# Optimization experiments

Measured on AMD Instinct MI355X. Metric: run time of the kernel, lower is better.

Reference implementation:

```python
import jax, jax.numpy as jnp
import numpy as np

D_MODEL = 2048
N_HEADS = 32
N_KV = 8
HEAD_DIM = D_MODEL // N_HEADS        # 64
N_GROUPS = N_HEADS // N_KV           # 4
ROPE_BASE = 10000.0
SCALE = HEAD_DIM ** -0.5
BATCH, SEQ = 2, 2048


def setup_inputs() -> dict:
    key = jax.random.key(0)
    k1, k2, k3, k4, k5 = jax.random.split(key, 5)
    init = 0.02  # typical transformer init scale
    return {
        "x":  jax.random.normal(k1, (BATCH, SEQ, D_MODEL), jnp.float32),
        "Wq": jax.random.normal(k2, (D_MODEL, D_MODEL), jnp.float32) * init,
        "Wk": jax.random.normal(k3, (N_KV * HEAD_DIM, D_MODEL), jnp.float32) * init,
        "Wv": jax.random.normal(k4, (N_KV * HEAD_DIM, D_MODEL), jnp.float32) * init,
        "Wo": jax.random.normal(k5, (D_MODEL, D_MODEL), jnp.float32) * init,
    }


def _apply_rope(q, k, seq_len):
    # q: (b, n_heads, s, hd), k: (b, n_kv, s, hd). LLaMA-style rotate-half RoPE.
    half = HEAD_DIM // 2
    inv_freq = 1.0 / (ROPE_BASE ** (jnp.arange(0, half, dtype=jnp.float32) / half))
    ang = jnp.arange(seq_len, dtype=jnp.float32)[:, None] * inv_freq[None, :]  # (s, half)
    cos = jnp.concatenate([jnp.cos(ang), jnp.cos(ang)], axis=-1)[None, None]   # (1,1,s,hd)
    sin = jnp.concatenate([jnp.sin(ang), jnp.sin(ang)], axis=-1)[None, None]

    def rot_half(t):
        t1, t2 = jnp.split(t, 2, axis=-1)
        return jnp.concatenate([-t2, t1], axis=-1)

    q = q * cos + rot_half(q) * sin
    k = k * cos + rot_half(k) * sin
    return q, k


def reference(x, Wq, Wk, Wv, Wo):
    b, s, _ = x.shape
    # projections (nn.Linear: y = x @ W.T)
    q = jnp.einsum('bsd,ed->bse', x, Wq).reshape(b, s, N_HEADS, HEAD_DIM).transpose(0, 2, 1, 3)
    k = jnp.einsum('bsd,ed->bse', x, Wk).reshape(b, s, N_KV, HEAD_DIM).transpose(0, 2, 1, 3)
    v = jnp.einsum('bsd,ed->bse', x, Wv).reshape(b, s, N_KV, HEAD_DIM).transpose(0, 2, 1, 3)

    q, k = _apply_rope(q, k, s)

    # GQA: repeat_interleave(k, n_groups) maps q-head h -> kv-head h // n_groups,
    # equivalent to grouping consecutive q heads and broadcasting kv per group.
    qg = q.reshape(b, N_KV, N_GROUPS, s, HEAD_DIM)
    scores = jnp.einsum('bkgqd,bkld->bkgql', qg, k) * SCALE   # (b, n_kv, g, s, s)
    attn = jax.nn.softmax(scores, axis=-1)
    out = jnp.einsum('bkgql,bkld->bkgqd', attn, v)            # (b, n_kv, g, s, hd)

    out = out.reshape(b, N_HEADS, s, HEAD_DIM).transpose(0, 2, 1, 3).reshape(b, s, D_MODEL)
    return jnp.einsum('bsd,ed->bse', out, Wo)
```

## Files before the change

### kernel.cpp

```cpp
#include <hip/hip_runtime.h>
#include <hip/hip_bf16.h>


typedef __attribute__((ext_vector_type(8))) short short8;
typedef __attribute__((ext_vector_type(4))) float f32x4;
typedef __attribute__((ext_vector_type(16))) float f32x16;

#define MFMA16(A, B, C) __builtin_amdgcn_mfma_f32_16x16x32_bf16((A), (B), (C), 0, 0, 0)
#define MFMA32(A, B, C) __builtin_amdgcn_mfma_f32_32x32x16_bf16((A), (B), (C), 0, 0, 0)

__device__ __forceinline__ ushort f2bf(float f) {
  __hip_bfloat16 h = __float2bfloat16(f);
  return __builtin_bit_cast(ushort, h);
}

__device__ __forceinline__ void gload_lds16(const void* g, void* l) {
  __builtin_amdgcn_global_load_lds(
      (const __attribute__((address_space(1))) unsigned int*)g,
      (__attribute__((address_space(3))) unsigned int*)l, 16, 0, 0);
}

__global__ __launch_bounds__(256) void prep_kernel(
    const float* __restrict__ x, const float* __restrict__ Wq,
    const float* __restrict__ Wk, const float* __restrict__ Wv,
    const float* __restrict__ Wo, ushort* __restrict__ xbf,
    ushort* __restrict__ wqbf, ushort* __restrict__ wkbf,
    ushort* __restrict__ wvbf, ushort* __restrict__ wobf,
    float* __restrict__ tc, float* __restrict__ ts) {
  const int blk = blockIdx.x;
  if (blk < 9216) {
    const float* src;
    ushort* dst;
    int t;
    if (blk < 4096) {
      src = x; dst = xbf; t = blk * 256 + threadIdx.x;
    } else if (blk < 6144) {
      src = Wq; dst = wqbf; t = (blk - 4096) * 256 + threadIdx.x;
    } else if (blk < 6656) {
      src = Wk; dst = wkbf; t = (blk - 6144) * 256 + threadIdx.x;
    } else if (blk < 7168) {
      src = Wv; dst = wvbf; t = (blk - 6656) * 256 + threadIdx.x;
    } else {
      src = Wo; dst = wobf; t = (blk - 7168) * 256 + threadIdx.x;
    }
    const float4* p = (const float4*)src;
    float4 a = p[t * 2], b = p[t * 2 + 1];
    int4 o;
    o.x = (int)f2bf(a.x) | ((int)f2bf(a.y) << 16);
    o.y = (int)f2bf(a.z) | ((int)f2bf(a.w) << 16);
    o.z = (int)f2bf(b.x) | ((int)f2bf(b.y) << 16);
    o.w = (int)f2bf(b.z) | ((int)f2bf(b.w) << 16);
    ((int4*)dst)[t] = o;
  } else {
    int t = (blk - 9216) * 256 + threadIdx.x;
    int j = t & 31, s = t >> 5;
    float freq = powf(10000.0f, -(float)j * (1.0f / 32.0f));
    float ang = (float)s * freq;
    tc[t] = cosf(ang);
    ts[t] = sinf(ang);
  }
}

__device__ __forceinline__ void gemm_core(const ushort* __restrict__ A,
                                          const ushort* __restrict__ Bt,
                                          int row0, int col0, int K,
                                          f32x4 (&acc)[4][4]) {
  __shared__ __align__(16) ushort As[8192];
  __shared__ __align__(16) ushort Bs[8192];
  const int t = threadIdx.x;
  const int lane = t & 63, wid = t >> 6;
  const int lr = lane & 15, lh = lane >> 4;
  const int wm = wid >> 1, wn = wid & 1;
#pragma unroll
  for (int i = 0; i < 4; ++i)
#pragma unroll
    for (int j = 0; j < 4; ++j) acc[i][j] = (f32x4){0.f, 0.f, 0.f, 0.f};

  const int srow = t >> 3, scg = (t & 7) ^ (srow & 7);
  const ushort* Asrc = A + (size_t)(row0 + srow) * K + scg * 8;
  const ushort* Bsrc = Bt + (size_t)(col0 + srow) * K + scg * 8;
  char* AsB = (char*)As + wid * 1024;
  char* BsB = (char*)Bs + wid * 1024;
  const int s7a = lr & 7;

  for (int k0 = 0; k0 < K; k0 += 64) {
    __syncthreads();
#pragma unroll
    for (int i = 0; i < 4; ++i) {
      gload_lds16(Asrc + (size_t)(32 * i) * K + k0, AsB + i * 4096);
      gload_lds16(Bsrc + (size_t)(32 * i) * K + k0, BsB + i * 4096);
    }
    __syncthreads();

    short8 af[4][2];
#pragma unroll
    for (int fm = 0; fm < 4; ++fm)
#pragma unroll
      for (int kk = 0; kk < 2; ++kk)
        af[fm][kk] = *(const short8*)((const char*)As +
                                      ((wm * 64 + fm * 16 + lr) << 7) +
                                      (((kk * 4 + lh) ^ s7a) << 4));
#pragma unroll
    for (int kk = 0; kk < 2; ++kk)
#pragma unroll
      for (int fn = 0; fn < 4; ++fn) {
        short8 bf_ = *(const short8*)((const char*)Bs +
                                      ((wn * 64 + fn * 16 + lr) << 7) +
                                      (((kk * 4 + lh) ^ s7a) << 4));
#pragma unroll
        for (int fm = 0; fm < 4; ++fm)
          acc[fm][fn] = MFMA16(af[fm][kk], bf_, acc[fm][fn]);
      }
  }
}

__global__ __launch_bounds__(256) void gemm_qkv_kernel(
    const ushort* __restrict__ xbf, const ushort* __restrict__ wq,
    const ushort* __restrict__ wk, const ushort* __restrict__ wv,
    ushort* __restrict__ Qo, ushort* __restrict__ Ko, ushort* __restrict__ Vo,
    const float* __restrict__ tabc, const float* __restrict__ tabs) {
  int bx = blockIdx.x % 24, by = blockIdx.x / 24;
  const ushort* Bt;
  int cb;
  if (bx < 16) {
    Bt = wq; cb = bx;
  } else if (bx < 20) {
    Bt = wk; cb = bx - 16;
  } else {
    Bt = wv; cb = bx - 20;
  }
  f32x4 acc[4][4];
  gemm_core(xbf, Bt, by * 128, cb * 128, 2048, acc);

  const int lane = threadIdx.x & 63, wid = threadIdx.x >> 6;
  const int lr = lane & 15, lh = lane >> 4;
  const int wm = wid >> 1, wn = wid & 1;
  const int srow0 = by * 128 + wm * 64 + lh * 4;

  if (bx >= 20) {
    const int kv = cb * 2 + wn;
#pragma unroll
    for (int fm = 0; fm < 4; ++fm) {
      int srow = srow0 + fm * 16;
      int bb = srow >> 11, s = srow & 2047;
#pragma unroll
      for (int fn = 0; fn < 4; ++fn) {
        int d = fn * 16 + lr;
        ushort4 o;
        o.x = f2bf(acc[fm][fn][0]);
        o.y = f2bf(acc[fm][fn][1]);
        o.z = f2bf(acc[fm][fn][2]);
        o.w = f2bf(acc[fm][fn][3]);
        *(ushort4*)&Vo[((size_t)((bb * 8 + kv) * 64 + d)) * 2048 + s] = o;
      }
    }
  } else {
    ushort* dst;
    int nh, h;
    float scale;
    if (bx < 16) {
      dst = Qo; nh = 32; h = bx * 2 + wn;
      scale = 0.125f * 1.44269504088896340736f;
    } else {
      dst = Ko; nh = 8; h = cb * 2 + wn; scale = 1.0f;
    }
#pragma unroll
    for (int fm = 0; fm < 4; ++fm) {
      int srow = srow0 + fm * 16;
      int bb = srow >> 11, sbase = srow & 2047;
      size_t obase = (size_t)(bb * nh + h) * 2048;
#pragma unroll
      for (int fn = 0; fn < 2; ++fn) {
        int j = fn * 16 + lr;
#pragma unroll
        for (int r = 0; r < 4; ++r) {
          int s = sbase + r;
          float c = tabc[s * 32 + j], sn = tabs[s * 32 + j];
          float x1 = acc[fm][fn][r], x2 = acc[fm][fn + 2][r];
          ushort* po = &dst[(obase + s) * 64 + j];
          po[0] = f2bf((x1 * c - x2 * sn) * scale);
          po[32] = f2bf((x2 * c + x1 * sn) * scale);
        }
      }
    }
  }
}

__global__ __launch_bounds__(256) void gemm_o_kernel(const ushort* __restrict__ A,
                                                     const ushort* __restrict__ Wo,
                                                     float* __restrict__ C) {
  int bx = blockIdx.x & 15, by = blockIdx.x >> 4;
  int row0 = by * 128, col0 = bx * 128;
  f32x4 acc[4][4];
  gemm_core(A, Wo, row0, col0, 2048, acc);
  const int lane = threadIdx.x & 63, wid = threadIdx.x >> 6;
  const int lr = lane & 15, lh = lane >> 4;
  const int wm = wid >> 1, wn = wid & 1;
#pragma unroll
  for (int fm = 0; fm < 4; ++fm) {
    int r0 = row0 + wm * 64 + fm * 16 + lh * 4;
#pragma unroll
    for (int fn = 0; fn < 4; ++fn) {
      int cc = col0 + wn * 64 + fn * 16 + lr;
#pragma unroll
      for (int r = 0; r < 4; ++r) C[(size_t)(r0 + r) * 2048 + cc] = acc[fm][fn][r];
    }
  }
}

__global__ __launch_bounds__(256, 4) void attn_kernel(const ushort* __restrict__ Q,
                                                      const ushort* __restrict__ Kg,
                                                      const ushort* __restrict__ Vt,
                                                      ushort* __restrict__ O) {
  __shared__ __align__(16) char smem_c[32768];
  const int tid = threadIdx.x;
  const int lane = tid & 63;
  const int wid = tid >> 6;
  const int bid = ((blockIdx.x & 7) << 7) | (blockIdx.x >> 3);
  const int qp = bid & 63;
  const int kvh = (bid >> 6) & 7;
  const int b = bid >> 9;
  const int h = kvh * 4 + wid;
  const int q0 = qp * 32;
  const int l31 = lane & 31;
  const int hi = lane >> 5;

  const ushort* Qp = Q + ((size_t)((b * 32 + h) * 2048 + q0)) * 64;
  const ushort* Kp = Kg + ((size_t)((b * 8 + kvh) * 2048)) * 64;
  const ushort* Vp = Vt + ((size_t)((b * 8 + kvh) * 64)) * 2048;

  const int srow = tid >> 3, scg = (tid & 7) ^ (srow & 7);
  const ushort* Kst = Kp + (size_t)srow * 64 + scg * 8;
  const ushort* Vst = Vp + (size_t)srow * 2048 + scg * 8;

#define STAGE(PAR, KV0)                                                         \
  do {                                                                          \
    char* kd_ = smem_c + (PAR) * 8192 + wid * 1024;                             \
    char* vd_ = smem_c + 16384 + (PAR) * 8192 + wid * 1024;                     \
    gload_lds16(Kst + (size_t)(KV0) * 64, kd_);                                 \
    gload_lds16(Kst + (size_t)((KV0) + 32) * 64, kd_ + 4096);                   \
    gload_lds16(Vst + (KV0), vd_);                                              \
    gload_lds16(Vst + 32 * 2048 + (KV0), vd_ + 4096);                           \
  } while (0)

  STAGE(0, 0);

  const short8 qf0 = *(const short8*)(Qp + (size_t)l31 * 64 + 0 + hi * 8);
  const short8 qf1 = *(const short8*)(Qp + (size_t)l31 * 64 + 16 + hi * 8);
  const short8 qf2 = *(const short8*)(Qp + (size_t)l31 * 64 + 32 + hi * 8);
  const short8 qf3 = *(const short8*)(Qp + (size_t)l31 * 64 + 48 + hi * 8);

  const int s7 = l31 & 7;
  const int ok0 = l31 * 128 + (((0 + hi) ^ s7) << 4);
  const int ok1 = l31 * 128 + (((2 + hi) ^ s7) << 4);
  const int ok2 = l31 * 128 + (((4 + hi) ^ s7) << 4);
  const int ok3 = l31 * 128 + (((6 + hi) ^ s7) << 4);

  f32x16 acc0, acc1, kz;
#pragma unroll
  for (int r = 0; r < 16; ++r) {
    acc0[r] = 0.f;
    acc1[r] = 0.f;
    kz[r] = 0.f;
  }
  float lsh = 0.f;

#define QK(ST, KOFF)                                         \
  do {                                                       \
    const char* kb_ = smem_c + (KOFF);                       \
    short8 kf_ = *(const short8*)(kb_ + ok0);                \
    __builtin_amdgcn_s_setprio(1);                           \
    ST = MFMA32(kf_, qf0, kz);                               \
    kf_ = *(const short8*)(kb_ + ok1);                       \
    ST = MFMA32(kf_, qf1, ST);                               \
    kf_ = *(const short8*)(kb_ + ok2);                       \
    ST = MFMA32(kf_, qf2, ST);                               \
    kf_ = *(const short8*)(kb_ + ok3);                       \
    ST = MFMA32(kf_, qf3, ST);                               \
    __builtin_amdgcn_s_setprio(0);                           \
  } while (0)

#define SMPV(ST, VOFF, VSX)                                                   \
  do {                                                                        \
    float ps_ = 0.f;                                                          \
    uint pk0_, pk1_, pk2_, pk3_, pk4_, pk5_, pk6_, pk7_;                      \
    _Pragma("unroll") for (int j = 0; j < 8; ++j) {                           \
      float pa_ = exp2f(ST[2 * j]);                                           \
      float pb_ = exp2f(ST[2 * j + 1]);                                       \
      ps_ += pa_ + pb_;                                                       \
      uint w_ = __builtin_amdgcn_perm(__builtin_bit_cast(uint, pb_),          \
                                      __builtin_bit_cast(uint, pa_),          \
                                      0x07060302u);                           \
      switch (j) {                                                            \
        case 0: pk0_ = w_; break;                                             \
        case 1: pk1_ = w_; break;                                             \
        case 2: pk2_ = w_; break;                                             \
        case 3: pk3_ = w_; break;                                             \
        case 4: pk4_ = w_; break;                                             \
        case 5: pk5_ = w_; break;                                             \
        case 6: pk6_ = w_; break;                                             \
        default: pk7_ = w_; break;                                            \
      }                                                                       \
    }                                                                         \
    lsh += ps_;                                                               \
    uint u0_ = hi ? pk0_ : pk2_; u0_ = __shfl_xor(u0_, 32);                   \
    uint u1_ = hi ? pk1_ : pk3_; u1_ = __shfl_xor(u1_, 32);                   \
    uint u2_ = hi ? pk4_ : pk6_; u2_ = __shfl_xor(u2_, 32);                   \
    uint u3_ = hi ? pk5_ : pk7_; u3_ = __shfl_xor(u3_, 32);                   \
    union { uint u[4]; short8 s; } f0_, f1_;                                  \
    f0_.u[0] = hi ? u0_ : pk0_;                                               \
    f0_.u[1] = hi ? u1_ : pk1_;                                               \
    f0_.u[2] = hi ? pk2_ : u0_;                                               \
    f0_.u[3] = hi ? pk3_ : u1_;                                               \
    f1_.u[0] = hi ? u2_ : pk4_;                                               \
    f1_.u[1] = hi ? u3_ : pk5_;                                               \
    f1_.u[2] = hi ? pk6_ : u2_;                                               \
    f1_.u[3] = hi ? pk7_ : u3_;                                               \
    const char* vb_ = smem_c + (VOFF);                                        \
    short8 v0_ = *(const short8*)(vb_ + (ok0 ^ (VSX)));                       \
    short8 v1_ = *(const short8*)(vb_ + (ok1 ^ (VSX)));                       \
    __builtin_amdgcn_s_setprio(1);                                            \
    acc0 = MFMA32(v0_, f0_.s, acc0);                                          \
    acc0 = MFMA32(v1_, f1_.s, acc0);                                          \
    __builtin_amdgcn_s_setprio(0);                                            \
    v0_ = *(const short8*)(vb_ + (ok0 ^ (VSX)) + 4096);                       \
    v1_ = *(const short8*)(vb_ + (ok1 ^ (VSX)) + 4096);                       \
    __builtin_amdgcn_s_setprio(1);                                            \
    acc1 = MFMA32(v0_, f0_.s, acc1);                                          \
    acc1 = MFMA32(v1_, f1_.s, acc1);                                          \
    __builtin_amdgcn_s_setprio(0);                                            \
  } while (0)

  for (int t = 0; t < 32; ++t) {
    asm volatile("s_waitcnt vmcnt(0)" ::: "memory");
    __builtin_amdgcn_s_barrier();
    if (t < 31) STAGE((t + 1) & 1, (t + 1) * 64);
    {
      const int kb = (t & 1) * 8192;
      const int vb = 16384 + (t & 1) * 8192;
      f32x16 st0_, st1_;
      QK(st0_, kb);
      QK(st1_, kb + 4096);
      SMPV(st0_, vb, 0);
      SMPV(st1_, vb, 64);
    }
  }
#undef STAGE
#undef QK
#undef SMPV

  float ls = lsh + __shfl_xor(lsh, 32);
  float inv = 1.0f / ls;
  ushort* Ob = O + (size_t)(b * 2048 + q0 + l31) * 2048 + h * 64;
#pragma unroll
  for (int rg = 0; rg < 4; ++rg) {
    ushort4 o0, o1;
    o0.x = f2bf(acc0[rg * 4 + 0] * inv);
    o0.y = f2bf(acc0[rg * 4 + 1] * inv);
    o0.z = f2bf(acc0[rg * 4 + 2] * inv);
    o0.w = f2bf(acc0[rg * 4 + 3] * inv);
    o1.x = f2bf(acc1[rg * 4 + 0] * inv);
    o1.y = f2bf(acc1[rg * 4 + 1] * inv);
    o1.z = f2bf(acc1[rg * 4 + 2] * inv);
    o1.w = f2bf(acc1[rg * 4 + 3] * inv);
    *(ushort4*)(Ob + rg * 8 + hi * 4) = o0;
    *(ushort4*)(Ob + 32 + rg * 8 + hi * 4) = o1;
  }
}

extern "C" void kernel_launch(void* const* d_in, const int* in_sizes, int n_in,
                              void* d_out, int out_size, void* d_ws, size_t ws_size,
                              hipStream_t stream) {
  (void)in_sizes; (void)n_in; (void)out_size; (void)ws_size;
  const float* x = (const float*)d_in[0];
  const float* Wq = (const float*)d_in[1];
  const float* Wk = (const float*)d_in[2];
  const float* Wv = (const float*)d_in[3];
  const float* Wo = (const float*)d_in[4];
  float* out = (float*)d_out;

  char* ws = (char*)d_ws;
  size_t off = 0;
  auto take = [&](size_t bytes) {
    void* p = ws + off;
    off += (bytes + 255) & ~(size_t)255;
    return p;
  };
  ushort* xbf = (ushort*)take(16777216);
  ushort* wqbf = (ushort*)take(8388608);
  ushort* wkbf = (ushort*)take(2097152);
  ushort* wvbf = (ushort*)take(2097152);
  ushort* wobf = (ushort*)take(8388608);
  ushort* Qbf = (ushort*)take(16777216);
  ushort* Kbf = (ushort*)take(4194304);
  ushort* Vtb = (ushort*)take(4194304);
  ushort* attnout = (ushort*)take(16777216);
  float* tabc = (float*)take(262144);
  float* tabs = (float*)take(262144);

  prep_kernel<<<9472, 256, 0, stream>>>(x, Wq, Wk, Wv, Wo, xbf, wqbf, wkbf,
                                        wvbf, wobf, tabc, tabs);
  gemm_qkv_kernel<<<768, 256, 0, stream>>>(xbf, wqbf, wkbf, wvbf, Qbf, Kbf,
                                           Vtb, tabc, tabs);
  attn_kernel<<<1024, 256, 0, stream>>>(Qbf, Kbf, Vtb, attnout);
  gemm_o_kernel<<<512, 256, 0, stream>>>(attnout, wobf, out);
}
```

Measured before the change: 241.8 us.

## Process two 32-row query tiles per wave to reuse K/V tiles

Each attention block now covers 64 query rows instead of 32, so every wave keeps two sets of Q fragments and accumulators and reuses each K and V LDS fragment for both. This halves the grid and halves the K/V global-to-LDS staging per query row. In exchange register pressure roughly doubles, so launch bounds drop to 2 blocks per SM, cutting occupancy. The softmax exp2 also switches to the raw hardware exp instruction.

```diff
diff --git a/kernel.cpp b/kernel.cpp
--- a/kernel.cpp
+++ b/kernel.cpp
@@ -12,6 +12,16 @@
 __device__ __forceinline__ ushort f2bf(float f) {
   __hip_bfloat16 h = __float2bfloat16(f);
   return __builtin_bit_cast(ushort, h);
+}
+
+__device__ __forceinline__ float fexp2(float x) {
+#if __has_builtin(__builtin_amdgcn_exp2f)
+  return __builtin_amdgcn_exp2f(x);
+#else
+  float r;
+  asm("v_exp_f32 %0, %1" : "=v"(r) : "v"(x));
+  return r;
+#endif
 }
 
 __device__ __forceinline__ void gload_lds16(const void* g, void* l) {
@@ -208,7 +218,7 @@
   }
 }
 
-__global__ __launch_bounds__(256, 4) void attn_kernel(const ushort* __restrict__ Q,
+__global__ __launch_bounds__(256, 2) void attn_kernel(const ushort* __restrict__ Q,
                                                       const ushort* __restrict__ Kg,
                                                       const ushort* __restrict__ Vt,
                                                       ushort* __restrict__ O) {
@@ -216,12 +226,12 @@
   const int tid = threadIdx.x;
   const int lane = tid & 63;
   const int wid = tid >> 6;
-  const int bid = ((blockIdx.x & 7) << 7) | (blockIdx.x >> 3);
-  const int qp = bid & 63;
-  const int kvh = (bid >> 6) & 7;
-  const int b = bid >> 9;
+  const int bid = ((blockIdx.x & 7) << 6) | (blockIdx.x >> 3);
+  const int qp = bid & 31;
+  const int kvh = (bid >> 5) & 7;
+  const int b = bid >> 8;
   const int h = kvh * 4 + wid;
-  const int q0 = qp * 32;
+  const int q0 = qp * 64;
   const int l31 = lane & 31;
   const int hi = lane >> 5;
 
@@ -245,10 +255,14 @@
 
   STAGE(0, 0);
 
-  const short8 qf0 = *(const short8*)(Qp + (size_t)l31 * 64 + 0 + hi * 8);
-  const short8 qf1 = *(const short8*)(Qp + (size_t)l31 * 64 + 16 + hi * 8);
-  const short8 qf2 = *(const short8*)(Qp + (size_t)l31 * 64 + 32 + hi * 8);
-  const short8 qf3 = *(const short8*)(Qp + (size_t)l31 * 64 + 48 + hi * 8);
+  const short8 qfA0 = *(const short8*)(Qp + (size_t)l31 * 64 + 0 + hi * 8);
+  const short8 qfA1 = *(const short8*)(Qp + (size_t)l31 * 64 + 16 + hi * 8);
+  const short8 qfA2 = *(const short8*)(Qp + (size_t)l31 * 64 + 32 + hi * 8);
+  const short8 qfA3 = *(const short8*)(Qp + (size_t)l31 * 64 + 48 + hi * 8);
+  const short8 qfB0 = *(const short8*)(Qp + (size_t)(32 + l31) * 64 + 0 + hi * 8);
+  const short8 qfB1 = *(const short8*)(Qp + (size_t)(32 + l31) * 64 + 16 + hi * 8);
+  const short8 qfB2 = *(const short8*)(Qp + (size_t)(32 + l31) * 64 + 32 + hi * 8);
+  const short8 qfB3 = *(const short8*)(Qp + (size_t)(32 + l31) * 64 + 48 + hi * 8);
 
   const int s7 = l31 & 7;
   const int ok0 = l31 * 128 + (((0 + hi) ^ s7) << 4);
@@ -256,37 +270,43 @@
   const int ok2 = l31 * 128 + (((4 + hi) ^ s7) << 4);
   const int ok3 = l31 * 128 + (((6 + hi) ^ s7) << 4);
 
-  f32x16 acc0, acc1, kz;
+  f32x16 accA0, accA1, accB0, accB1, kz;
 #pragma unroll
   for (int r = 0; r < 16; ++r) {
-    acc0[r] = 0.f;
-    acc1[r] = 0.f;
+    accA0[r] = 0.f;
+    accA1[r] = 0.f;
+    accB0[r] = 0.f;
+    accB1[r] = 0.f;
     kz[r] = 0.f;
   }
-  float lsh = 0.f;
-
-#define QK(ST, KOFF)                                         \
+  float lshA = 0.f, lshB = 0.f;
+
+#define QK2(STA, STB, KOFF)                                  \
   do {                                                       \
     const char* kb_ = smem_c + (KOFF);                       \
     short8 kf_ = *(const short8*)(kb_ + ok0);                \
     __builtin_amdgcn_s_setprio(1);                           \
-    ST = MFMA32(kf_, qf0, kz);                               \
+    STA = MFMA32(kf_, qfA0, kz);                             \
+    STB = MFMA32(kf_, qfB0, kz);                             \
     kf_ = *(const short8*)(kb_ + ok1);                       \
-    ST = MFMA32(kf_, qf1, ST);                               \
+    STA = MFMA32(kf_, qfA1, STA);                            \
+    STB = MFMA32(kf_, qfB1, STB);                            \
     kf_ = *(const short8*)(kb_ + ok2);                       \
-    ST = MFMA32(kf_, qf2, ST);                               \
+    STA = MFMA32(kf_, qfA2, STA);                            \
+    STB = MFMA32(kf_, qfB2, STB);                            \
     kf_ = *(const short8*)(kb_ + ok3);                       \
-    ST = MFMA32(kf_, qf3, ST);                               \
+    STA = MFMA32(kf_, qfA3, STA);                            \
+    STB = MFMA32(kf_, qfB3, STB);                            \
     __builtin_amdgcn_s_setprio(0);                           \
   } while (0)
 
-#define SMPV(ST, VOFF, VSX)                                                   \
+#define SMX(ST, F0, F1, LSH)                                                  \
   do {                                                                        \
     float ps_ = 0.f;                                                          \
     uint pk0_, pk1_, pk2_, pk3_, pk4_, pk5_, pk6_, pk7_;                      \
     _Pragma("unroll") for (int j = 0; j < 8; ++j) {                           \
-      float pa_ = exp2f(ST[2 * j]);                                           \
-      float pb_ = exp2f(ST[2 * j + 1]);                                       \
+      float pa_ = fexp2(ST[2 * j]);                                           \
+      float pb_ = fexp2(ST[2 * j + 1]);                                       \
       ps_ += pa_ + pb_;                                                       \
       uint w_ = __builtin_amdgcn_perm(__builtin_bit_cast(uint, pb_),          \
                                       __builtin_bit_cast(uint, pa_),          \
@@ -302,33 +322,43 @@
         default: pk7_ = w_; break;                                            \
       }                                                                       \
     }                                                                         \
-    lsh += ps_;                                                               \
+    LSH += ps_;                                                               \
     uint u0_ = hi ? pk0_ : pk2_; u0_ = __shfl_xor(u0_, 32);                   \
     uint u1_ = hi ? pk1_ : pk3_; u1_ = __shfl_xor(u1_, 32);                   \
     uint u2_ = hi ? pk4_ : pk6_; u2_ = __shfl_xor(u2_, 32);                   \
     uint u3_ = hi ? pk5_ : pk7_; u3_ = __shfl_xor(u3_, 32);                   \
-    union { uint u[4]; short8 s; } f0_, f1_;                                  \
-    f0_.u[0] = hi ? u0_ : pk0_;                                               \
-    f0_.u[1] = hi ? u1_ : pk1_;                                               \
-    f0_.u[2] = hi ? pk2_ : u0_;                                               \
-    f0_.u[3] = hi ? pk3_ : u1_;                                               \
-    f1_.u[0] = hi ? u2_ : pk4_;                                               \
-    f1_.u[1] = hi ? u3_ : pk5_;                                               \
-    f1_.u[2] = hi ? pk6_ : u2_;                                               \
-    f1_.u[3] = hi ? pk7_ : u3_;                                               \
-    const char* vb_ = smem_c + (VOFF);                                        \
-    short8 v0_ = *(const short8*)(vb_ + (ok0 ^ (VSX)));                       \
-    short8 v1_ = *(const short8*)(vb_ + (ok1 ^ (VSX)));                       \
-    __builtin_amdgcn_s_setprio(1);                                            \
-    acc0 = MFMA32(v0_, f0_.s, acc0);                                          \
-    acc0 = MFMA32(v1_, f1_.s, acc0);                                          \
-    __builtin_amdgcn_s_setprio(0);                                            \
-    v0_ = *(const short8*)(vb_ + (ok0 ^ (VSX)) + 4096);                       \
-    v1_ = *(const short8*)(vb_ + (ok1 ^ (VSX)) + 4096);                       \
-    __builtin_amdgcn_s_setprio(1);                                            \
-    acc1 = MFMA32(v0_, f0_.s, acc1);                                          \
-    acc1 = MFMA32(v1_, f1_.s, acc1);                                          \
-    __builtin_amdgcn_s_setprio(0);                                            \
+    F0.u[0] = hi ? u0_ : pk0_;                                                \
+    F0.u[1] = hi ? u1_ : pk1_;                                                \
+    F0.u[2] = hi ? pk2_ : u0_;                                                \
+    F0.u[3] = hi ? pk3_ : u1_;                                                \
+    F1.u[0] = hi ? u2_ : pk4_;                                                \
+    F1.u[1] = hi ? u3_ : pk5_;                                                \
+    F1.u[2] = hi ? pk6_ : u2_;                                                \
+    F1.u[3] = hi ? pk7_ : u3_;                                                \
+  } while (0)
+
+#define SMPV2(STA, STB, VOFF, VSX)                                           \
+  do {                                                                       \
+    union { uint u[4]; short8 s; } fA0_, fA1_, fB0_, fB1_;                   \
+    SMX(STA, fA0_, fA1_, lshA);                                              \
+    SMX(STB, fB0_, fB1_, lshB);                                              \
+    const char* vb_ = smem_c + (VOFF);                                       \
+    short8 v0_ = *(const short8*)(vb_ + (ok0 ^ (VSX)));                      \
+    short8 v1_ = *(const short8*)(vb_ + (ok1 ^ (VSX)));                      \
+    __builtin_amdgcn_s_setprio(1);                                           \
+    accA0 = MFMA32(v0_, fA0_.s, accA0);                                      \
+    accA0 = MFMA32(v1_, fA1_.s, accA0);                                      \
+    accB0 = MFMA32(v0_, fB0_.s, accB0);                                      \
+    accB0 = MFMA32(v1_, fB1_.s, accB0);                                      \
+    __builtin_amdgcn_s_setprio(0);                                           \
+    v0_ = *(const short8*)(vb_ + (ok0 ^ (VSX)) + 4096);                      \
+    v1_ = *(const short8*)(vb_ + (ok1 ^ (VSX)) + 4096);                      \
+    __builtin_amdgcn_s_setprio(1);                                           \
+    accA1 = MFMA32(v0_, fA0_.s, accA1);                                      \
+    accA1 = MFMA32(v1_, fA1_.s, accA1);                                      \
+    accB1 = MFMA32(v0_, fB0_.s, accB1);                                      \
+    accB1 = MFMA32(v1_, fB1_.s, accB1);                                      \
+    __builtin_amdgcn_s_setprio(0);                                           \
   } while (0)
 
   for (int t = 0; t < 32; ++t) {
@@ -338,33 +368,47 @@
     {
       const int kb = (t & 1) * 8192;
       const int vb = 16384 + (t & 1) * 8192;
-      f32x16 st0_, st1_;
-      QK(st0_, kb);
-      QK(st1_, kb + 4096);
-      SMPV(st0_, vb, 0);
-      SMPV(st1_, vb, 64);
+      f32x16 stA0_, stB0_, stA1_, stB1_;
+      QK2(stA0_, stB0_, kb);
+      QK2(stA1_, stB1_, kb + 4096);
+      SMPV2(stA0_, stB0_, vb, 0);
+      SMPV2(stA1_, stB1_, vb, 64);
     }
   }
 #undef STAGE
-#undef QK
-#undef SMPV
-
-  float ls = lsh + __shfl_xor(lsh, 32);
-  float inv = 1.0f / ls;
-  ushort* Ob = O + (size_t)(b * 2048 + q0 + l31) * 2048 + h * 64;
+#undef QK2
+#undef SMX
+#undef SMPV2
+
+  const float lsA = lshA + __shfl_xor(lshA, 32);
+  const float lsB = lshB + __shfl_xor(lshB, 32);
+  const float invA = 1.0f / lsA;
+  const float invB = 1.0f / lsB;
+  ushort* ObA = O + (size_t)(b * 2048 + q0 + l31) * 2048 + h * 64;
+  ushort* ObB = O + (size_t)(b * 2048 + q0 + 32 + l31) * 2048 + h * 64;
 #pragma unroll
   for (int rg = 0; rg < 4; ++rg) {
     ushort4 o0, o1;
-    o0.x = f2bf(acc0[rg * 4 + 0] * inv);
-    o0.y = f2bf(acc0[rg * 4 + 1] * inv);
-    o0.z = f2bf(acc0[rg * 4 + 2] * inv);
-    o0.w = f2bf(acc0[rg * 4 + 3] * inv);
-    o1.x = f2bf(acc1[rg * 4 + 0] * inv);
-    o1.y = f2bf(acc1[rg * 4 + 1] * inv);
-    o1.z = f2bf(acc1[rg * 4 + 2] * inv);
-    o1.w = f2bf(acc1[rg * 4 + 3] * inv);
-    *(ushort4*)(Ob + rg * 8 + hi * 4) = o0;
-    *(ushort4*)(Ob + 32 + rg * 8 + hi * 4) = o1;
+    o0.x = f2bf(accA0[rg * 4 + 0] * invA);
+    o0.y = f2bf(accA0[rg * 4 + 1] * invA);
+    o0.z = f2bf(accA0[rg * 4 + 2] * invA);
+    o0.w = f2bf(accA0[rg * 4 + 3] * invA);
+    o1.x = f2bf(accA1[rg * 4 + 0] * invA);
+    o1.y = f2bf(accA1[rg * 4 + 1] * invA);
+    o1.z = f2bf(accA1[rg * 4 + 2] * invA);
+    o1.w = f2bf(accA1[rg * 4 + 3] * invA);
+    *(ushort4*)(ObA + rg * 8 + hi * 4) = o0;
+    *(ushort4*)(ObA + 32 + rg * 8 + hi * 4) = o1;
+    o0.x = f2bf(accB0[rg * 4 + 0] * invB);
+    o0.y = f2bf(accB0[rg * 4 + 1] * invB);
+    o0.z = f2bf(accB0[rg * 4 + 2] * invB);
+    o0.w = f2bf(accB0[rg * 4 + 3] * invB);
+    o1.x = f2bf(accB1[rg * 4 + 0] * invB);
+    o1.y = f2bf(accB1[rg * 4 + 1] * invB);
+    o1.z = f2bf(accB1[rg * 4 + 2] * invB);
+    o1.w = f2bf(accB1[rg * 4 + 3] * invB);
+    *(ushort4*)(ObB + rg * 8 + hi * 4) = o0;
+    *(ushort4*)(ObB + 32 + rg * 8 + hi * 4) = o1;
   }
 }
 
@@ -402,6 +446,6 @@
                                         wvbf, wobf, tabc, tabs);
   gemm_qkv_kernel<<<768, 256, 0, stream>>>(xbf, wqbf, wkbf, wvbf, Qbf, Kbf,
                                            Vtb, tabc, tabs);
-  attn_kernel<<<1024, 256, 0, stream>>>(Qbf, Kbf, Vtb, attnout);
+  attn_kernel<<<512, 256, 0, stream>>>(Qbf, Kbf, Vtb, attnout);
   gemm_o_kernel<<<512, 256, 0, stream>>>(attnout, wobf, out);
 }
```

New measurement: 209.1 us. 1.16x faster.
